# Kernel optimization log

Hardware: AMD Instinct MI355X
Metric: run time of the kernel (lower is better)

The kernel has to match this reference:

```python
import jax, jax.numpy as jnp
import numpy as np
import math

D_MODEL = 1024
N_HEADS = 16
HEAD_DIM = D_MODEL // N_HEADS
B = 2
S = 2048

def setup_inputs() -> dict:
    key = jax.random.key(0)
    ks = jax.random.split(key, 5)
    x = jax.random.normal(ks[0], (B, S, D_MODEL), dtype=jnp.float32)
    # causal lower-triangular mask, broadcastable to [B, H, S, S]
    mask = jnp.tril(jnp.ones((S, S), dtype=bool))[None, None, :, :]
    # qkv_proj: Linear(d_model, 3*d_model); out_proj: Linear(d_model, d_model)
    lim_qkv = 1.0 / math.sqrt(D_MODEL)
    Wqkv = jax.random.uniform(ks[1], (D_MODEL, 3 * D_MODEL), minval=-lim_qkv, maxval=lim_qkv, dtype=jnp.float32)
    bqkv = jax.random.uniform(ks[2], (3 * D_MODEL,), minval=-lim_qkv, maxval=lim_qkv, dtype=jnp.float32)
    Wo = jax.random.uniform(ks[3], (D_MODEL, D_MODEL), minval=-lim_qkv, maxval=lim_qkv, dtype=jnp.float32)
    bo = jax.random.uniform(ks[4], (D_MODEL,), minval=-lim_qkv, maxval=lim_qkv, dtype=jnp.float32)
    return {"x": x, "mask": mask, "Wqkv": Wqkv, "bqkv": bqkv, "Wo": Wo, "bo": bo}

def reference(x, mask, Wqkv, bqkv, Wo, bo):
    b, s, d = x.shape
    scale = math.sqrt(HEAD_DIM)
    qkv = x @ Wqkv + bqkv                                   # [b, s, 3d]
    qkv = qkv.reshape(b, s, 3, N_HEADS, HEAD_DIM)
    qkv = jnp.transpose(qkv, (2, 0, 3, 1, 4))               # [3, b, h, s, hd]
    q, k, v = qkv[0], qkv[1], qkv[2]
    scores = jnp.einsum("bhqd,bhkd->bhqk", q, k) / scale    # [b, h, s, s]
    scores = jnp.where(mask, scores, -jnp.inf)
    attn = jax.nn.softmax(scores, axis=-1)                  # dropout inactive (eval)
    out = jnp.einsum("bhqk,bhkd->bhqd", attn, v)            # [b, h, s, hd]
    out = jnp.transpose(out, (0, 2, 1, 3)).reshape(b, s, d)
    return out @ Wo + bo
```

## Files before the change

### kernel.cpp

```cpp
#include <hip/hip_runtime.h>
#include <stdint.h>

typedef __bf16 bf16x8 __attribute__((ext_vector_type(8)));
typedef __bf16 bf16x4 __attribute__((ext_vector_type(4)));
typedef short  s16x4  __attribute__((ext_vector_type(4)));
typedef float  f32x4  __attribute__((ext_vector_type(4)));

#if __has_builtin(__builtin_amdgcn_mfma_f32_16x16x16_bf16)
#define HAVE_MFMA16 2
#elif __has_builtin(__builtin_amdgcn_mfma_f32_16x16x16bf16_1k)
#define HAVE_MFMA16 1
#else
#define HAVE_MFMA16 0
#endif

__device__ __forceinline__ float bf2f(ushort u) {
    union { uint i; float f; } v; v.i = ((uint)u) << 16; return v.f;
}
__device__ __forceinline__ ushort f2bf(float f) {
    union { uint i; float f; } v; v.f = f;
    uint i = v.i;
    uint r = (i + 0x7fffu + ((i >> 16) & 1u)) >> 16;
    return (ushort)r;
}
__device__ __forceinline__ ushort f2bf_t(float f) {
    union { uint i; float f; } v; v.f = f;
    return (ushort)(v.i >> 16);
}
__device__ __forceinline__ uint pack_bf2(float a, float b) {
    union { uint i; float f; } va, vb; va.f = a; vb.f = b;
    return (va.i >> 16) | (vb.i & 0xffff0000u);
}

#if HAVE_MFMA16
__device__ __forceinline__ f32x4 mfma16(uint2 a, uint2 b, f32x4 c) {
#if HAVE_MFMA16 == 2
    return __builtin_amdgcn_mfma_f32_16x16x16_bf16(*(bf16x4*)&a, *(bf16x4*)&b, c, 0, 0, 0);
#else
    return __builtin_amdgcn_mfma_f32_16x16x16bf16_1k(*(s16x4*)&a, *(s16x4*)&b, c, 0, 0, 0);
#endif
}
#endif

#if __has_builtin(__builtin_amdgcn_exp2f)
#define EXP2F __builtin_amdgcn_exp2f
#else
#define EXP2F exp2f
#endif

__device__ __forceinline__ void gld16(const ushort* g, ushort* l) {
    __builtin_amdgcn_global_load_lds((const __attribute__((address_space(1))) uint*)g,
                                     (__attribute__((address_space(3))) uint*)l, 16, 0, 0);
}

#define D_MODEL 1024
#define N_HEADS 16
#define HEAD_DIM 64
#define BATCH 2
#define SEQ 2048
#define M_ROWS (BATCH * SEQ)
#define N_ITEMS 1024
#define SCALE_LOG2E 0.18033688f

__global__ __launch_bounds__(256) void cast_f32_bf16(
    const float* __restrict__ in, ushort* __restrict__ out, int n4)
{
    int i = blockIdx.x * 256 + threadIdx.x;
    if (i < n4) {
        float4 v = ((const float4*)in)[i];
        ushort4 o;
        o.x = f2bf(v.x); o.y = f2bf(v.y); o.z = f2bf(v.z); o.w = f2bf(v.w);
        ((ushort4*)out)[i] = o;
    }
}

__global__ __launch_bounds__(256) void transpose_f32_bf16(
    const float* __restrict__ in, ushort* __restrict__ out, int K, int N)
{
    __shared__ float tile[64][65];
    const int k0 = blockIdx.y << 6, n0 = blockIdx.x << 6;
    const int tid = threadIdx.x;
    {
        const int r  = tid >> 4;
        const int c4 = (tid & 15) * 4;
#pragma unroll
        for (int rr = 0; rr < 4; ++rr) {
            int kk = r + rr * 16;
            float4 v = *(const float4*)(in + (size_t)(k0 + kk) * N + n0 + c4);
            tile[kk][c4 + 0] = v.x; tile[kk][c4 + 1] = v.y;
            tile[kk][c4 + 2] = v.z; tile[kk][c4 + 3] = v.w;
        }
    }
    __syncthreads();
    {
        const int nn = tid & 63;
        const int ch = tid >> 6;
#pragma unroll
        for (int cc = 0; cc < 2; ++cc) {
            int k8 = (ch + cc * 4) * 8;
            ushort tmp[8] __attribute__((aligned(16)));
#pragma unroll
            for (int j = 0; j < 8; ++j) tmp[j] = f2bf(tile[k8 + j][nn]);
            *(uint4*)(out + (size_t)(n0 + nn) * K + k0 + k8) = *(const uint4*)tmp;
        }
    }
}

__global__ __launch_bounds__(256) void gemm_bt128(
    const ushort* __restrict__ A, const ushort* __restrict__ Bt,
    const float* __restrict__ bias, float* __restrict__ out,
    ushort* __restrict__ Qb, ushort* __restrict__ Kb, ushort* __restrict__ Vb,
    int M, int N, int K, int mode)
{
    __shared__ ushort smem[64 * 136];
    ushort* As = smem;
    ushort* Bs = smem + 128 * 32;
    const int tid = threadIdx.x, lane = tid & 63, w = tid >> 6;
    const int wr = w >> 1, wc = w & 1;
    const int m0 = blockIdx.y * 128, n0 = blockIdx.x * 128;
    const int quad = lane >> 4, r15 = lane & 15, q8 = quad * 8;

    f32x4 acc[4][4] = {};

    const int cb0 = w * 64;
    const int cb1 = 256 + w * 64;
    const int c0 = cb0 + lane, c1 = cb1 + lane;
    const int row0 = c0 >> 2, sc0 = (c0 & 3) * 8;
    const int row1 = c1 >> 2, sc1 = (c1 & 3) * 8;

    for (int k0 = 0; k0 < K; k0 += 32) {
        gld16(A  + (size_t)(m0 + row0) * K + k0 + sc0, As + cb0 * 8);
        gld16(A  + (size_t)(m0 + row1) * K + k0 + sc1, As + cb1 * 8);
        gld16(Bt + (size_t)(n0 + row0) * K + k0 + sc0, Bs + cb0 * 8);
        gld16(Bt + (size_t)(n0 + row1) * K + k0 + sc1, Bs + cb1 * 8);
        __syncthreads();
        bf16x8 af[4], bfv[4];
#pragma unroll
        for (int mt = 0; mt < 4; ++mt)
            af[mt] = *(const bf16x8*)&As[(wr * 64 + mt * 16 + r15) * 32 + q8];
#pragma unroll
        for (int nt = 0; nt < 4; ++nt)
            bfv[nt] = *(const bf16x8*)&Bs[(wc * 64 + nt * 16 + r15) * 32 + q8];
#pragma unroll
        for (int mt = 0; mt < 4; ++mt)
#pragma unroll
            for (int nt = 0; nt < 4; ++nt)
                acc[mt][nt] = __builtin_amdgcn_mfma_f32_16x16x32_bf16(af[mt], bfv[nt], acc[mt][nt], 0, 0, 0);
        __syncthreads();
    }

    const int q4 = quad * 4;
    float bv[4];
#pragma unroll
    for (int nt = 0; nt < 4; ++nt) bv[nt] = bias[n0 + wc * 64 + nt * 16 + r15];

    if (mode == 0) {
        ushort* Cs = smem;
#pragma unroll
        for (int h = 0; h < 2; ++h) {
            __syncthreads();
            if (wr == h) {
#pragma unroll
                for (int mt = 0; mt < 4; ++mt)
#pragma unroll
                    for (int nt = 0; nt < 4; ++nt)
#pragma unroll
                        for (int r = 0; r < 4; ++r)
                            Cs[(mt * 16 + q4 + r) * 136 + wc * 64 + nt * 16 + r15] =
                                f2bf(acc[mt][nt][r] + bv[nt]);
            }
            __syncthreads();
#pragma unroll
            for (int it = 0; it < 4; ++it) {
                int idx = it * 256 + tid;
                int row = idx >> 4, chunk = idx & 15;
                int m = m0 + h * 64 + row;
                int n = n0 + chunk * 8;
                int which = n >> 10, nh = n & 1023;
                int hh = nh >> 6, d = nh & 63;
                int b = m >> 11, s = m & 2047;
                size_t dst = (((size_t)(b * N_HEADS + hh)) * SEQ + s) * HEAD_DIM + d;
                ushort* p = (which == 0) ? Qb : ((which == 1) ? Kb : Vb);
                *(uint4*)(p + dst) = *(const uint4*)&Cs[row * 136 + chunk * 8];
            }
        }
    } else {
        float* Cf = (float*)smem;
#pragma unroll
        for (int h = 0; h < 4; ++h) {
            __syncthreads();
            if (wr == (h >> 1)) {
                const int mtb = (h & 1) * 2;
#pragma unroll
                for (int mt2 = 0; mt2 < 2; ++mt2)
#pragma unroll
                    for (int nt = 0; nt < 4; ++nt)
#pragma unroll
                        for (int r = 0; r < 4; ++r)
                            Cf[(mt2 * 16 + q4 + r) * 136 + wc * 64 + nt * 16 + r15] =
                                acc[mtb + mt2][nt][r] + bv[nt];
            }
            __syncthreads();
#pragma unroll
            for (int it = 0; it < 4; ++it) {
                int idx = it * 256 + tid;
                int row = idx >> 5, chunk = idx & 31;
                float4 v = *(const float4*)&Cf[row * 136 + chunk * 4];
                int m = m0 + h * 32 + row;
                *(float4*)(out + (size_t)m * N + n0 + chunk * 4) = v;
            }
        }
    }
}

__global__ __launch_bounds__(256) void attn_mfma(
    const ushort* __restrict__ Q, const ushort* __restrict__ K,
    const ushort* __restrict__ V, ushort* __restrict__ Out,
    int* __restrict__ counter)
{
    __shared__ ushort Ks[2][64 * 72];
    __shared__ ushort Vt[2][64 * 72];
#if !HAVE_MFMA16
    __shared__ ushort Ps[4][16 * 72];
#endif
    __shared__ int s_item;

    const int tid  = threadIdx.x;
    const int lane = tid & 63;
    const int w    = tid >> 6;
    const int quad = lane >> 4;
    const int r15  = lane & 15;
    const int q8   = quad * 8;

    const int srow = tid >> 2;
    const int scol = (tid & 3) * 16;
    const int kp = tid & 31;
    const int dg = tid >> 5;

    for (;;) {
        __syncthreads();
        if (tid == 0) s_item = atomicAdd(counter, 1);
        __syncthreads();
        const int item = s_item;
        if (item >= N_ITEMS) break;

        const int qblk = 31 - (item >> 5);
        const int bh   = item & 31;
        const int q0   = qblk * 64;
        const size_t base = (size_t)bh * SEQ * HEAD_DIM;
        const int wq0  = q0 + w * 16;
        const int ntiles = qblk + 1;

        bf16x8 qf[2];
        {
            const ushort* qrow = Q + base + (size_t)(wq0 + r15) * HEAD_DIM;
            qf[0] = *(const bf16x8*)(qrow + q8);
            qf[1] = *(const bf16x8*)(qrow + 32 + q8);
        }

        f32x4 o_acc[4] = {};
#if HAVE_MFMA16
        float l_sc = 0.f;
#else
        float l_lane[4] = {0.f, 0.f, 0.f, 0.f};
#endif

        uint4 kr0, kr1, vr0, vr1;
        {
            const ushort* kpt = K + base + (size_t)srow * HEAD_DIM + scol;
            kr0 = *(const uint4*)kpt; kr1 = *(const uint4*)(kpt + 8);
            const ushort* vpt = V + base + (size_t)(2 * kp) * HEAD_DIM + dg * 8;
            vr0 = *(const uint4*)vpt; vr1 = *(const uint4*)(vpt + HEAD_DIM);
        }
        {
            ushort* ks = &Ks[0][0];
            *(uint4*)&ks[srow * 72 + scol]     = kr0;
            *(uint4*)&ks[srow * 72 + scol + 8] = kr1;
            const ushort* a = (const ushort*)&vr0;
            const ushort* b = (const ushort*)&vr1;
            uint* vt32 = (uint*)&Vt[0][0];
#pragma unroll
            for (int j = 0; j < 8; ++j)
                vt32[(dg * 8 + j) * 36 + ((kp + 4 * dg) & 31)] = (uint)a[j] | ((uint)b[j] << 16);
        }
        if (ntiles > 1) {
            const ushort* kpt = K + base + (size_t)(64 + srow) * HEAD_DIM + scol;
            kr0 = *(const uint4*)kpt; kr1 = *(const uint4*)(kpt + 8);
            const ushort* vpt = V + base + (size_t)(64 + 2 * kp) * HEAD_DIM + dg * 8;
            vr0 = *(const uint4*)vpt; vr1 = *(const uint4*)(vpt + HEAD_DIM);
        }

        for (int t = 0; t < ntiles; ++t) {
            __syncthreads();
            if (t + 1 < ntiles) {
                const int b1 = (t + 1) & 1;
                ushort* ks = &Ks[b1][0];
                *(uint4*)&ks[srow * 72 + scol]     = kr0;
                *(uint4*)&ks[srow * 72 + scol + 8] = kr1;
                const ushort* a = (const ushort*)&vr0;
                const ushort* b = (const ushort*)&vr1;
                uint* vt32 = (uint*)&Vt[b1][0];
#pragma unroll
                for (int j = 0; j < 8; ++j)
                    vt32[(dg * 8 + j) * 36 + ((kp + 4 * dg) & 31)] = (uint)a[j] | ((uint)b[j] << 16);
            }
            if (t + 2 < ntiles) {
                const int key2 = (t + 2) << 6;
                const ushort* kpt = K + base + (size_t)(key2 + srow) * HEAD_DIM + scol;
                kr0 = *(const uint4*)kpt; kr1 = *(const uint4*)(kpt + 8);
                const ushort* vpt = V + base + (size_t)(key2 + 2 * kp) * HEAD_DIM + dg * 8;
                vr0 = *(const uint4*)vpt; vr1 = *(const uint4*)(vpt + HEAD_DIM);
            }

            const ushort* KsB = &Ks[t & 1][0];
            const ushort* VtB = &Vt[t & 1][0];
            const bool diag = (t == ntiles - 1);
            const int ntmax = diag ? (w + 1) : 4;

#if HAVE_MFMA16
            f32x4 s_acc[4];
            __builtin_amdgcn_s_setprio(1);
#pragma unroll
            for (int nt = 0; nt < 4; ++nt) {
                if (nt >= ntmax) continue;
                f32x4 z = {};
#pragma unroll
                for (int ks = 0; ks < 2; ++ks) {
                    bf16x8 kf = *(const bf16x8*)&KsB[(nt * 16 + r15) * 72 + ks * 32 + q8];
                    z = __builtin_amdgcn_mfma_f32_16x16x32_bf16(kf, qf[ks], z, 0, 0, 0);
                }
                s_acc[nt] = z;
            }
            __builtin_amdgcn_s_setprio(0);
            uint2 pa[4];
#pragma unroll
            for (int nt = 0; nt < 4; ++nt) {
                if (nt >= ntmax) continue;
#pragma unroll
                for (int j = 0; j < 4; ++j) {
                    float e = EXP2F(s_acc[nt][j] * SCALE_LOG2E);
                    if (diag && nt == w && quad * 4 + j > r15) e = 0.f;
                    s_acc[nt][j] = e;
                    l_sc += e;
                }
                pa[nt].x = pack_bf2(s_acc[nt][0], s_acc[nt][1]);
                pa[nt].y = pack_bf2(s_acc[nt][2], s_acc[nt][3]);
            }
            __builtin_amdgcn_s_setprio(1);
            const uint* vt32 = (const uint*)VtB;
#pragma unroll
            for (int ds = 0; ds < 4; ++ds) {
                const int d = ds * 16 + r15;
                const int rowb = d * 36 + ((4 * (d >> 3)) & 31);
#pragma unroll
                for (int nt = 0; nt < 4; ++nt) {
                    if (nt >= ntmax) continue;
                    const int cw = (nt * 8 + quad * 2 + 4 * (d >> 3)) & 31;
                    uint2 vb = *(const uint2*)&vt32[d * 36 + cw];
                    o_acc[ds] = mfma16(pa[nt], vb, o_acc[ds]);
                }
            }
            __builtin_amdgcn_s_setprio(0);
#else
            f32x4 s_acc[4];
            __builtin_amdgcn_s_setprio(1);
#pragma unroll
            for (int nt = 0; nt < 4; ++nt) {
                if (nt >= ntmax) continue;
                f32x4 z = {};
#pragma unroll
                for (int ks = 0; ks < 2; ++ks) {
                    bf16x8 kf = *(const bf16x8*)&KsB[(nt * 16 + r15) * 72 + ks * 32 + q8];
                    z = __builtin_amdgcn_mfma_f32_16x16x32_bf16(qf[ks], kf, z, 0, 0, 0);
                }
                s_acc[nt] = z;
            }
            __builtin_amdgcn_s_setprio(0);
#pragma unroll
            for (int nt = 0; nt < 4; ++nt) {
                if (nt >= ntmax) continue;
#pragma unroll
                for (int j = 0; j < 4; ++j) {
                    float e = EXP2F(s_acc[nt][j] * SCALE_LOG2E);
                    if (diag && nt == w && r15 > quad * 4 + j) e = 0.f;
                    s_acc[nt][j] = e;
                    l_lane[j] += e;
                }
            }
            ushort* pb = &Ps[w][0];
#pragma unroll
            for (int nt = 0; nt < 4; ++nt)
#pragma unroll
                for (int j = 0; j < 4; ++j)
                    pb[(quad * 4 + j) * 72 + nt * 16 + r15] =
                        (nt < ntmax) ? f2bf_t(s_acc[nt][j]) : (ushort)0;
            bf16x8 pf0 = *(const bf16x8*)&pb[r15 * 72 + q8];
            bf16x8 pf1 = *(const bf16x8*)&pb[r15 * 72 + 32 + q8];

            __builtin_amdgcn_s_setprio(1);
#pragma unroll
            for (int nt = 0; nt < 4; ++nt) {
                const int d0 = nt * 16 + r15;
                const int dsw = 4 * ((d0 >> 3) & 7);
                const int c0 = (4 * quad + dsw) & 31;
                const int c1 = (16 + 4 * quad + dsw) & 31;
                bf16x8 vf0 = *(const bf16x8*)&VtB[d0 * 72 + (c0 << 1)];
                bf16x8 vf1 = *(const bf16x8*)&VtB[d0 * 72 + (c1 << 1)];
                o_acc[nt] = __builtin_amdgcn_mfma_f32_16x16x32_bf16(pf0, vf0, o_acc[nt], 0, 0, 0);
                o_acc[nt] = __builtin_amdgcn_mfma_f32_16x16x32_bf16(pf1, vf1, o_acc[nt], 0, 0, 0);
            }
            __builtin_amdgcn_s_setprio(0);
#endif
        }

        float l_f[4];
#if HAVE_MFMA16
        float lt = l_sc + __shfl_xor(l_sc, 16);
        lt += __shfl_xor(lt, 32);
#pragma unroll
        for (int j = 0; j < 4; ++j) {
            float lq = __shfl(lt, (lane & 48) | (quad * 4 + j));
            l_f[j] = 1.f / lq;
        }
#else
#pragma unroll
        for (int j = 0; j < 4; ++j) {
            float l = l_lane[j];
            l += __shfl_xor(l, 1);
            l += __shfl_xor(l, 2);
            l += __shfl_xor(l, 4);
            l += __shfl_xor(l, 8);
            l_f[j] = 1.f / l;
        }
#endif
        const int b = bh >> 4, h = bh & 15;
#pragma unroll
        for (int nt = 0; nt < 4; ++nt) {
#pragma unroll
            for (int j = 0; j < 4; ++j) {
                int qg = wq0 + quad * 4 + j;
                float v = o_acc[nt][j] * l_f[j];
                Out[((size_t)(b * SEQ + qg)) * D_MODEL + h * 64 + nt * 16 + r15] = f2bf(v);
            }
        }
    }
}

extern "C" void kernel_launch(void* const* d_in, const int* in_sizes, int n_in,
                              void* d_out, int out_size, void* d_ws, size_t ws_size,
                              hipStream_t stream)
{
    const float* x    = (const float*)d_in[0];
    const float* Wqkv = (const float*)d_in[2];
    const float* bqkv = (const float*)d_in[3];
    const float* Wo   = (const float*)d_in[4];
    const float* bo   = (const float*)d_in[5];
    float* out = (float*)d_out;

    char* ws = (char*)d_ws;
    size_t off = 0;
    ushort* xb    = (ushort*)(ws + off); off += (size_t)M_ROWS * D_MODEL * 2;
    ushort* WqkvT = (ushort*)(ws + off); off += (size_t)3 * D_MODEL * D_MODEL * 2;
    ushort* WoT   = (ushort*)(ws + off); off += (size_t)D_MODEL * D_MODEL * 2;
    const size_t qkv_elems = (size_t)BATCH * N_HEADS * SEQ * HEAD_DIM;
    ushort* Qb = (ushort*)(ws + off); off += qkv_elems * 2;
    ushort* Kb = (ushort*)(ws + off); off += qkv_elems * 2;
    ushort* Vb = (ushort*)(ws + off); off += qkv_elems * 2;
    ushort* attn_out = (ushort*)(ws + off); off += (size_t)M_ROWS * D_MODEL * 2;
    int* counter = (int*)(ws + off); off += 256;

    hipMemsetAsync(counter, 0, 4, stream);

    {
        int n4 = M_ROWS * D_MODEL / 4;
        cast_f32_bf16<<<(n4 + 255) / 256, 256, 0, stream>>>(x, xb, n4);
    }

    transpose_f32_bf16<<<dim3(3 * D_MODEL / 64, D_MODEL / 64), 256, 0, stream>>>(Wqkv, WqkvT, D_MODEL, 3 * D_MODEL);
    transpose_f32_bf16<<<dim3(D_MODEL / 64, D_MODEL / 64), 256, 0, stream>>>(Wo, WoT, D_MODEL, D_MODEL);

    gemm_bt128<<<dim3(3 * D_MODEL / 128, M_ROWS / 128), 256, 0, stream>>>(
        xb, WqkvT, bqkv, nullptr, Qb, Kb, Vb, M_ROWS, 3 * D_MODEL, D_MODEL, 0);

    attn_mfma<<<1024, 256, 0, stream>>>(Qb, Kb, Vb, attn_out, counter);

    gemm_bt128<<<dim3(D_MODEL / 128, M_ROWS / 128), 256, 0, stream>>>(
        attn_out, WoT, bo, out, nullptr, nullptr, nullptr, M_ROWS, D_MODEL, D_MODEL, 1);
}
```

Measured before the change: 221.5 us.

## Split long causal query blocks across two KV ranges with a combine kernel

Query blocks 16–31 of the causal attention are split into two work items covering different key-tile ranges, and the items are ordered so that long and short ones pair up for load balance across the persistent grid. The unnormalized partial outputs and row sums go to workspace in fp32, and a new combine kernel adds them and normalizes. The aim is to shorten the tail caused by the longest diagonal blocks, at the cost of extra fp32 global traffic, an extra launch, and a workspace-size dependency (it falls back to the old path when the workspace is too small). Because the kernel skips the max subtraction, the partials share a scale and can be added directly.

```diff
diff --git a/kernel.cpp b/kernel.cpp
--- a/kernel.cpp
+++ b/kernel.cpp
@@ -59,7 +59,6 @@
 #define BATCH 2
 #define SEQ 2048
 #define M_ROWS (BATCH * SEQ)
-#define N_ITEMS 1024
 #define SCALE_LOG2E 0.18033688f
 
 __global__ __launch_bounds__(256) void cast_f32_bf16(
@@ -216,7 +215,8 @@
 __global__ __launch_bounds__(256) void attn_mfma(
     const ushort* __restrict__ Q, const ushort* __restrict__ K,
     const ushort* __restrict__ V, ushort* __restrict__ Out,
-    int* __restrict__ counter)
+    float* __restrict__ Opart, float* __restrict__ Lpart,
+    int* __restrict__ counter, int n_items, int split)
 {
     __shared__ ushort Ks[2][64 * 72];
     __shared__ ushort Vt[2][64 * 72];
@@ -242,14 +242,30 @@
         if (tid == 0) s_item = atomicAdd(counter, 1);
         __syncthreads();
         const int item = s_item;
-        if (item >= N_ITEMS) break;
-
-        const int qblk = 31 - (item >> 5);
-        const int bh   = item & 31;
+        if (item >= n_items) break;
+
+        const int bh = item & 31;
+        int qblk, t0k, t1k;
+        if (split) {
+            const int c = item >> 5;
+            if (c < 2)        { qblk = 31;     t0k = c * 16; t1k = t0k + 16; }
+            else if (c < 17)  { qblk = 32 - c; t0k = 0;      t1k = 16; }
+            else if (c == 17) { qblk = 15;     t0k = 0;      t1k = 16; }
+            else {
+                const int r = c - 18, s = 15 - (r >> 1);
+                if ((r & 1) == 0) { qblk = 15 + s; t0k = 16; t1k = 16 + s; }
+                else              { qblk = s - 1;  t0k = 0;  t1k = s; }
+            }
+        } else {
+            qblk = 31 - (item >> 5); t0k = 0; t1k = qblk + 1;
+        }
+        const int ntiles = qblk + 1;
+        const int two_part = split && (qblk >= 16);
+        const int part = (t0k == 0) ? 0 : 1;
+
         const int q0   = qblk * 64;
         const size_t base = (size_t)bh * SEQ * HEAD_DIM;
         const int wq0  = q0 + w * 16;
-        const int ntiles = qblk + 1;
 
         bf16x8 qf[2];
         {
@@ -267,32 +283,32 @@
 
         uint4 kr0, kr1, vr0, vr1;
         {
-            const ushort* kpt = K + base + (size_t)srow * HEAD_DIM + scol;
+            const ushort* kpt = K + base + (size_t)((t0k << 6) + srow) * HEAD_DIM + scol;
             kr0 = *(const uint4*)kpt; kr1 = *(const uint4*)(kpt + 8);
-            const ushort* vpt = V + base + (size_t)(2 * kp) * HEAD_DIM + dg * 8;
+            const ushort* vpt = V + base + (size_t)((t0k << 6) + 2 * kp) * HEAD_DIM + dg * 8;
             vr0 = *(const uint4*)vpt; vr1 = *(const uint4*)(vpt + HEAD_DIM);
         }
         {
-            ushort* ks = &Ks[0][0];
+            ushort* ks = &Ks[t0k & 1][0];
             *(uint4*)&ks[srow * 72 + scol]     = kr0;
             *(uint4*)&ks[srow * 72 + scol + 8] = kr1;
             const ushort* a = (const ushort*)&vr0;
             const ushort* b = (const ushort*)&vr1;
-            uint* vt32 = (uint*)&Vt[0][0];
+            uint* vt32 = (uint*)&Vt[t0k & 1][0];
 #pragma unroll
             for (int j = 0; j < 8; ++j)
                 vt32[(dg * 8 + j) * 36 + ((kp + 4 * dg) & 31)] = (uint)a[j] | ((uint)b[j] << 16);
         }
-        if (ntiles > 1) {
-            const ushort* kpt = K + base + (size_t)(64 + srow) * HEAD_DIM + scol;
+        if (t0k + 1 < t1k) {
+            const ushort* kpt = K + base + (size_t)(((t0k + 1) << 6) + srow) * HEAD_DIM + scol;
             kr0 = *(const uint4*)kpt; kr1 = *(const uint4*)(kpt + 8);
-            const ushort* vpt = V + base + (size_t)(64 + 2 * kp) * HEAD_DIM + dg * 8;
+            const ushort* vpt = V + base + (size_t)(((t0k + 1) << 6) + 2 * kp) * HEAD_DIM + dg * 8;
             vr0 = *(const uint4*)vpt; vr1 = *(const uint4*)(vpt + HEAD_DIM);
         }
 
-        for (int t = 0; t < ntiles; ++t) {
+        for (int t = t0k; t < t1k; ++t) {
             __syncthreads();
-            if (t + 1 < ntiles) {
+            if (t + 1 < t1k) {
                 const int b1 = (t + 1) & 1;
                 ushort* ks = &Ks[b1][0];
                 *(uint4*)&ks[srow * 72 + scol]     = kr0;
@@ -304,7 +320,7 @@
                 for (int j = 0; j < 8; ++j)
                     vt32[(dg * 8 + j) * 36 + ((kp + 4 * dg) & 31)] = (uint)a[j] | ((uint)b[j] << 16);
             }
-            if (t + 2 < ntiles) {
+            if (t + 2 < t1k) {
                 const int key2 = (t + 2) << 6;
                 const ushort* kpt = K + base + (size_t)(key2 + srow) * HEAD_DIM + scol;
                 kr0 = *(const uint4*)kpt; kr1 = *(const uint4*)(kpt + 8);
@@ -351,7 +367,6 @@
 #pragma unroll
             for (int ds = 0; ds < 4; ++ds) {
                 const int d = ds * 16 + r15;
-                const int rowb = d * 36 + ((4 * (d >> 3)) & 31);
 #pragma unroll
                 for (int nt = 0; nt < 4; ++nt) {
                     if (nt >= ntmax) continue;
@@ -413,16 +428,39 @@
 #endif
         }
 
-        float l_f[4];
 #if HAVE_MFMA16
         float lt = l_sc + __shfl_xor(l_sc, 16);
         lt += __shfl_xor(lt, 32);
-#pragma unroll
-        for (int j = 0; j < 4; ++j) {
-            float lq = __shfl(lt, (lane & 48) | (quad * 4 + j));
-            l_f[j] = 1.f / lq;
+        if (two_part) {
+            const int slot = ((bh << 4) + (qblk - 16)) * 2 + part;
+            float* Op = Opart + (size_t)slot * 4096;
+            float* Lp = Lpart + (size_t)slot * 64;
+            if (lane < 16) Lp[w * 16 + lane] = lt;
+            const int rbase = w * 16 + quad * 4;
+#pragma unroll
+            for (int nt = 0; nt < 4; ++nt)
+#pragma unroll
+                for (int j = 0; j < 4; ++j)
+                    Op[(rbase + j) * 64 + nt * 16 + r15] = o_acc[nt][j];
+        } else {
+            float l_f[4];
+#pragma unroll
+            for (int j = 0; j < 4; ++j) {
+                float lq = __shfl(lt, (lane & 48) | (quad * 4 + j));
+                l_f[j] = 1.f / lq;
+            }
+            const int b = bh >> 4, h = bh & 15;
+#pragma unroll
+            for (int nt = 0; nt < 4; ++nt)
+#pragma unroll
+                for (int j = 0; j < 4; ++j) {
+                    int qg = wq0 + quad * 4 + j;
+                    float v = o_acc[nt][j] * l_f[j];
+                    Out[((size_t)(b * SEQ + qg)) * D_MODEL + h * 64 + nt * 16 + r15] = f2bf(v);
+                }
         }
 #else
+        float l_red[4];
 #pragma unroll
         for (int j = 0; j < 4; ++j) {
             float l = l_lane[j];
@@ -430,19 +468,64 @@
             l += __shfl_xor(l, 2);
             l += __shfl_xor(l, 4);
             l += __shfl_xor(l, 8);
-            l_f[j] = 1.f / l;
-        }
-#endif
-        const int b = bh >> 4, h = bh & 15;
-#pragma unroll
-        for (int nt = 0; nt < 4; ++nt) {
-#pragma unroll
-            for (int j = 0; j < 4; ++j) {
-                int qg = wq0 + quad * 4 + j;
-                float v = o_acc[nt][j] * l_f[j];
-                Out[((size_t)(b * SEQ + qg)) * D_MODEL + h * 64 + nt * 16 + r15] = f2bf(v);
-            }
-        }
+            l_red[j] = l;
+        }
+        if (two_part) {
+            const int slot = ((bh << 4) + (qblk - 16)) * 2 + part;
+            float* Op = Opart + (size_t)slot * 4096;
+            float* Lp = Lpart + (size_t)slot * 64;
+            const int rbase = w * 16 + quad * 4;
+            if (r15 == 0) {
+#pragma unroll
+                for (int j = 0; j < 4; ++j) Lp[rbase + j] = l_red[j];
+            }
+#pragma unroll
+            for (int nt = 0; nt < 4; ++nt)
+#pragma unroll
+                for (int j = 0; j < 4; ++j)
+                    Op[(rbase + j) * 64 + nt * 16 + r15] = o_acc[nt][j];
+        } else {
+            const int b = bh >> 4, h = bh & 15;
+#pragma unroll
+            for (int nt = 0; nt < 4; ++nt)
+#pragma unroll
+                for (int j = 0; j < 4; ++j) {
+                    int qg = wq0 + quad * 4 + j;
+                    float v = o_acc[nt][j] / l_red[j];
+                    Out[((size_t)(b * SEQ + qg)) * D_MODEL + h * 64 + nt * 16 + r15] = f2bf(v);
+                }
+        }
+#endif
+    }
+}
+
+__global__ __launch_bounds__(256) void attn_combine(
+    const float* __restrict__ Opart, const float* __restrict__ Lpart,
+    ushort* __restrict__ Out)
+{
+    const int sp = blockIdx.x;
+    const int bh = sp >> 4, qb16 = sp & 15;
+    const int qblk = 16 + qb16;
+    const int b = bh >> 4, h = bh & 15;
+    const float* O0 = Opart + (size_t)(sp * 2 + 0) * 4096;
+    const float* O1 = Opart + (size_t)(sp * 2 + 1) * 4096;
+    const float* L0 = Lpart + (size_t)(sp * 2 + 0) * 64;
+    const float* L1 = Lpart + (size_t)(sp * 2 + 1) * 64;
+    const int tid = threadIdx.x;
+#pragma unroll
+    for (int c = 0; c < 4; ++c) {
+        int e = c * 1024 + tid * 4;
+        int row = e >> 6, d = e & 63;
+        float4 a = *(const float4*)(O0 + e);
+        float4 bb = *(const float4*)(O1 + e);
+        float li = 1.f / (L0[row] + L1[row]);
+        ushort4 o;
+        o.x = f2bf((a.x + bb.x) * li);
+        o.y = f2bf((a.y + bb.y) * li);
+        o.z = f2bf((a.z + bb.z) * li);
+        o.w = f2bf((a.w + bb.w) * li);
+        int qg = qblk * 64 + row;
+        *(ushort4*)&Out[((size_t)(b * SEQ + qg)) * D_MODEL + h * 64 + d] = o;
     }
 }
 
@@ -468,6 +551,10 @@
     ushort* Vb = (ushort*)(ws + off); off += qkv_elems * 2;
     ushort* attn_out = (ushort*)(ws + off); off += (size_t)M_ROWS * D_MODEL * 2;
     int* counter = (int*)(ws + off); off += 256;
+    float* Opart = (float*)(ws + off); off += (size_t)32 * 16 * 2 * 4096 * 4;
+    float* Lpart = (float*)(ws + off); off += (size_t)32 * 16 * 2 * 64 * 4;
+    const int split = (off <= ws_size) ? 1 : 0;
+    const int n_items = split ? 1536 : 1024;
 
     hipMemsetAsync(counter, 0, 4, stream);
 
@@ -482,7 +569,10 @@
     gemm_bt128<<<dim3(3 * D_MODEL / 128, M_ROWS / 128), 256, 0, stream>>>(
         xb, WqkvT, bqkv, nullptr, Qb, Kb, Vb, M_ROWS, 3 * D_MODEL, D_MODEL, 0);
 
-    attn_mfma<<<1024, 256, 0, stream>>>(Qb, Kb, Vb, attn_out, counter);
+    attn_mfma<<<1024, 256, 0, stream>>>(Qb, Kb, Vb, attn_out, Opart, Lpart,
+                                        counter, n_items, split);
+    if (split)
+        attn_combine<<<512, 256, 0, stream>>>(Opart, Lpart, attn_out);
 
     gemm_bt128<<<dim3(D_MODEL / 128, M_ROWS / 128), 256, 0, stream>>>(
         attn_out, WoT, bo, out, nullptr, nullptr, nullptr, M_ROWS, D_MODEL, D_MODEL, 1);
```

Measured after the change: 242.7 us. 9.6% more time.
